# Performance work log

Measured on AMD Instinct MI355X. Metric: run time of the kernel, lower is better.

## Reference

```python
import jax, jax.numpy as jnp
import numpy as np

BN_EPS = 1e-5

@jax.custom_vjp
def bsign(x):
    # forward: sign(x) (torch semantics: sign(0)=0, matched by jnp.sign)
    return jnp.sign(x)

def _bsign_fwd(x):
    return jnp.sign(x), x

def _bsign_bwd(x, g):
    # straight-through estimator: pass grad where |x| <= 1, zero elsewhere
    return (g * (jnp.abs(x) <= 1.0).astype(g.dtype),)

bsign.defvjp(_bsign_fwd, _bsign_bwd)


def setup_inputs() -> dict:
    key = jax.random.key(0)
    k1, k2 = jax.random.split(key, 2)
    B, IN, OUT = 8192, 2048, 2048
    x = jax.random.normal(k1, (B, IN), dtype=jnp.float32)
    weight = jax.random.normal(k2, (OUT, IN), dtype=jnp.float32) * 0.1
    gamma = jnp.ones((OUT,), dtype=jnp.float32)
    beta = jnp.zeros((OUT,), dtype=jnp.float32)
    return {"x": x, "weight": weight, "gamma": gamma, "beta": beta}


def reference(x, weight, gamma, beta):
    # binarize input and weight to {-1, 0, +1} via sign (STE in bwd)
    xb = bsign(x)            # [B, IN]
    wb = bsign(weight)       # [OUT, IN]
    out = xb @ wb.T          # [B, OUT] full-precision GEMM over +/-1 values
    # BatchNorm1d, training mode: normalize with biased batch statistics
    mean = jnp.mean(out, axis=0)                 # [OUT]
    var = jnp.var(out, axis=0)                   # biased (ddof=0), matches torch BN
    out = (out - mean) * jax.lax.rsqrt(var + BN_EPS) * gamma + beta
    return out
```

## Files before the change

kernel.cpp:

```cpp
#include <hip/hip_runtime.h>
#include <stdint.h>


typedef int int32x4 __attribute__((ext_vector_type(4)));
typedef int int32x16 __attribute__((ext_vector_type(16)));

#define BM 256
#define BN 256
#define BKI 128
#define EPS_BN 1e-5f
#define BAR_STRIDE 32

__device__ __forceinline__ void load16_lds(const void* g, void* l) {
  __builtin_amdgcn_global_load_lds(
      (const __attribute__((address_space(1))) void*)g,
      (__attribute__((address_space(3))) void*)l,
      16, 0, 0);
}

__device__ __forceinline__ char sgn(float v) {
  return v > 0.f ? (char)1 : (v < 0.f ? (char)-1 : (char)0);
}

__global__ void binarize_kernel(const float* __restrict__ x,
                                const float* __restrict__ w,
                                char* __restrict__ Ab, char* __restrict__ Bb,
                                float* __restrict__ stats,
                                int nx4, int ntot4, int n2) {
  int idx = blockIdx.x * blockDim.x + threadIdx.x;
  if (idx < n2) stats[idx] = 0.f;
  if (idx >= ntot4) return;
  const float4* src;
  char* dst;
  int i;
  if (idx < nx4) {
    src = reinterpret_cast<const float4*>(x); dst = Ab; i = idx;
  } else {
    src = reinterpret_cast<const float4*>(w); dst = Bb; i = idx - nx4;
  }
  float4 v = src[i];
  char4 o;
  o.x = sgn(v.x); o.y = sgn(v.y); o.z = sgn(v.z); o.w = sgn(v.w);
  reinterpret_cast<char4*>(dst)[i] = o;
}

__global__ __launch_bounds__(512, 2) void gemm_bn_kernel(
    const char* __restrict__ A,
    const char* __restrict__ Bt,
    float* __restrict__ C,
    float* __restrict__ colSum,
    float* __restrict__ colSq,
    int* __restrict__ barriers,
    const float* __restrict__ gamma,
    const float* __restrict__ beta,
    int M, int N, int K) {
  __shared__ __align__(16) char sA[2][BM * BKI];
  __shared__ __align__(16) char sB[2][BN * BKI];

  const int tid  = threadIdx.x;
  const int wave = tid >> 6;
  const int lane = tid & 63;

  const int nby = M / BM;
  const int panel = blockIdx.x / nby;
  const int rowBlock = (blockIdx.x % nby) * BM;
  const int colBlock = panel * BN;

  const int laneRow = lane >> 3;
  const int cch     = lane & 7;
  int swzj[4];
#pragma unroll
  for (int j = 0; j < 4; ++j) swzj[j] = ((cch ^ laneRow ^ j) & 7) * 16;

  const char* Ag = A  + (size_t)(rowBlock + wave * 32 + laneRow) * K;
  const char* Bg = Bt + (size_t)(colBlock + wave * 32 + laneRow) * K;

  const int lane31 = lane & 31;
  const int hi     = lane >> 5;
  const int r2     = (lane31 >> 3) & 3;
  const int wm = (wave >> 2) * 128;
  const int wn = (wave & 3) * 64;

  int32x16 acc[4][2] = {};

  const int NT = K / BKI;

#pragma unroll
  for (int j = 0; j < 4; ++j) {
    load16_lds(Ag + (size_t)(j * 8) * K + swzj[j],
               &sA[0][(wave * 32 + j * 8) * BKI]);
    load16_lds(Bg + (size_t)(j * 8) * K + swzj[j],
               &sB[0][(wave * 32 + j * 8) * BKI]);
  }

  for (int t = 0; t < NT; ++t) {
    const int cur = t & 1;
    const int nxt = cur ^ 1;
    const char* sAc = sA[cur];
    const char* sBc = sB[cur];
    const size_t gkn = (size_t)(t + 1) * BKI;
    const bool pre = (t + 1 < NT);

    __syncthreads();

    int32x16 bf_[2];
    int32x4* bfv = reinterpret_cast<int32x4*>(&bf_[0]);
#pragma unroll
    for (int ni = 0; ni < 2; ++ni) {
      const int row = wn + ni * 32 + lane31;
#pragma unroll
      for (int ks = 0; ks < 4; ++ks) {
        const int chunk = (((ks * 2 + hi) ^ (row & 7) ^ r2) & 7) * 16;
        bfv[ni * 4 + ks] = *reinterpret_cast<const int32x4*>(
            &sBc[row * BKI + chunk]);
      }
    }

#pragma unroll
    for (int q = 0; q < 4; ++q) {
      int32x4 af[4];
      const int arow = wm + q * 32 + lane31;
#pragma unroll
      for (int ks = 0; ks < 4; ++ks) {
        const int chunk = (((ks * 2 + hi) ^ (arow & 7) ^ r2) & 7) * 16;
        af[ks] = *reinterpret_cast<const int32x4*>(&sAc[arow * BKI + chunk]);
      }

      if (pre) {
        if (q < 2) {
#pragma unroll
          for (int j = 0; j < 2; ++j) {
            const int part = q * 2 + j;
            load16_lds(Ag + gkn + (size_t)(part * 8) * K + swzj[part],
                       &sA[nxt][(wave * 32 + part * 8) * BKI]);
          }
        } else {
#pragma unroll
          for (int j = 0; j < 2; ++j) {
            const int part = (q - 2) * 2 + j;
            load16_lds(Bg + gkn + (size_t)(part * 8) * K + swzj[part],
                       &sB[nxt][(wave * 32 + part * 8) * BKI]);
          }
        }
      }

      __builtin_amdgcn_s_barrier();
      __builtin_amdgcn_s_setprio(1);
#pragma unroll
      for (int ks = 0; ks < 4; ++ks)
#pragma unroll
        for (int ni = 0; ni < 2; ++ni)
          acc[q][ni] = __builtin_amdgcn_mfma_i32_32x32x32_i8(
              af[ks], bfv[ni * 4 + ks], acc[q][ni], 0, 0, 0);
      __builtin_amdgcn_s_setprio(0);
      __builtin_amdgcn_s_barrier();
    }
  }

#pragma unroll
  for (int ni = 0; ni < 2; ++ni) {
    const int col = colBlock + wn + ni * 32 + lane31;
    float s = 0.f, sq = 0.f;
#pragma unroll
    for (int mi = 0; mi < 4; ++mi)
#pragma unroll
      for (int r = 0; r < 16; ++r) {
        const float fv = (float)acc[mi][ni][r];
        s += fv;
        sq += fv * fv;
      }
    s  += __shfl_xor(s, 32);
    sq += __shfl_xor(sq, 32);
    if (hi == 0) {
      atomicAdd(&colSum[col], s);
      atomicAdd(&colSq[col], sq);
    }
  }

  float gmv = 0.f, btv = 0.f;
  if (tid < BN) {
    gmv = gamma[colBlock + tid];
    btv = beta[colBlock + tid];
  }

  __syncthreads();
  if (tid == 0) {
    int* bar = barriers + panel * BAR_STRIDE;
    __hip_atomic_fetch_add(bar, 1, __ATOMIC_RELAXED,
                           __HIP_MEMORY_SCOPE_AGENT);
    while (__hip_atomic_load(bar, __ATOMIC_RELAXED,
                             __HIP_MEMORY_SCOPE_AGENT) < nby) {
      __builtin_amdgcn_s_sleep(8);
    }
    asm volatile("" ::: "memory");
  }
  __syncthreads();

  float2* sSC = reinterpret_cast<float2*>(&sA[0][0]);
  if (tid < BN) {
    const int col = colBlock + tid;
    const float s  = __hip_atomic_load(&colSum[col], __ATOMIC_RELAXED,
                                       __HIP_MEMORY_SCOPE_AGENT);
    const float sq = __hip_atomic_load(&colSq[col], __ATOMIC_RELAXED,
                                       __HIP_MEMORY_SCOPE_AGENT);
    const float invM = 1.0f / (float)M;
    const float mu  = s * invM;
    const float var = sq * invM - mu * mu;
    const float sc  = gmv * rsqrtf(var + EPS_BN);
    const float sh  = btv - mu * sc;
    sSC[tid] = make_float2(sc, sh);
  }
  __syncthreads();

#pragma unroll
  for (int ni = 0; ni < 2; ++ni) {
    const int lc  = wn + ni * 32 + lane31;
    const float2 ss = sSC[lc];
    const int col = colBlock + lc;
#pragma unroll
    for (int mi = 0; mi < 4; ++mi) {
#pragma unroll
      for (int r = 0; r < 16; ++r) {
        const int row = rowBlock + wm + mi * 32 + (r & 3) + 8 * (r >> 2) +
                        4 * hi;
        C[(size_t)row * N + col] = (float)acc[mi][ni][r] * ss.x + ss.y;
      }
    }
  }
}

extern "C" void kernel_launch(void* const* d_in, const int* in_sizes, int n_in,
                              void* d_out, int out_size, void* d_ws,
                              size_t ws_size, hipStream_t stream) {
  const float* x     = (const float*)d_in[0];
  const float* w     = (const float*)d_in[1];
  const float* gamma = (const float*)d_in[2];
  const float* beta  = (const float*)d_in[3];
  float* C = (float*)d_out;

  const int N = in_sizes[2];
  const int K = in_sizes[1] / N;
  const int M = in_sizes[0] / K;

  char* ws = (char*)d_ws;
  char* Abin = ws;
  char* Bbin = ws + (size_t)M * K;
  float* stats = (float*)(ws + (size_t)M * K + (size_t)N * K);
  float* colSum = stats;
  float* colSq  = stats + N;
  int* barriers = (int*)(stats + 2 * N);

  {
    int nx4 = (M * K) / 4;
    int ntot4 = (M * K + N * K) / 4;
    binarize_kernel<<<(ntot4 + 255) / 256, 256, 0, stream>>>(
        x, w, Abin, Bbin, stats, nx4, ntot4, 2 * N + 16 * BAR_STRIDE);
  }

  {
    const int nTiles = (M / BM) * (N / BN);
    gemm_bn_kernel<<<nTiles, 512, 0, stream>>>(Abin, Bbin, C, colSum, colSq,
                                               barriers, gamma, beta, M, N, K);
  }
}
```

Before: 161.8 us.

## Pack signs as FP4 and use scaled FP4 MFMA for binary GEMM

Binarization now packs eight sign values into a 32-bit word as e2m1 FP4 codes instead of int8 bytes. The GEMM uses the gfx950 scaled f8f6f4 MFMA in FP4 mode with unit scales and fp32 accumulation, halving the K-loop iterations and operand traffic. Results stay exact since sums of ±1 fit in fp32, at the cost of depending on the fp4 operand layout being right.

Measured after the change: 149.8 us. 1.08x faster.

```diff
diff --git a/kernel.cpp b/kernel.cpp
--- a/kernel.cpp
+++ b/kernel.cpp
@@ -3,13 +3,15 @@
 
 
 typedef int int32x4 __attribute__((ext_vector_type(4)));
-typedef int int32x16 __attribute__((ext_vector_type(16)));
+typedef int int32x8 __attribute__((ext_vector_type(8)));
+typedef float f32x16 __attribute__((ext_vector_type(16)));
 
 #define BM 256
 #define BN 256
 #define BKI 128
 #define EPS_BN 1e-5f
 #define BAR_STRIDE 32
+#define SCALE_ONE 0x7F7F7F7F
 
 __device__ __forceinline__ void load16_lds(const void* g, void* l) {
   __builtin_amdgcn_global_load_lds(
@@ -18,30 +20,39 @@
       16, 0, 0);
 }
 
-__device__ __forceinline__ char sgn(float v) {
-  return v > 0.f ? (char)1 : (v < 0.f ? (char)-1 : (char)0);
+__device__ __forceinline__ int32x8 mk8(int32x4 v) {
+  int32x8 r = {v[0], v[1], v[2], v[3], 0, 0, 0, 0};
+  return r;
+}
+
+__device__ __forceinline__ unsigned enc4(float v) {
+  return v > 0.f ? 2u : (v < 0.f ? 10u : 0u);
 }
 
 __global__ void binarize_kernel(const float* __restrict__ x,
                                 const float* __restrict__ w,
-                                char* __restrict__ Ab, char* __restrict__ Bb,
+                                unsigned* __restrict__ Ab,
+                                unsigned* __restrict__ Bb,
                                 float* __restrict__ stats,
-                                int nx4, int ntot4, int n2) {
+                                int nx8, int ntot8, int n2) {
   int idx = blockIdx.x * blockDim.x + threadIdx.x;
   if (idx < n2) stats[idx] = 0.f;
-  if (idx >= ntot4) return;
+  if (idx >= ntot8) return;
   const float4* src;
-  char* dst;
+  unsigned* dst;
   int i;
-  if (idx < nx4) {
+  if (idx < nx8) {
     src = reinterpret_cast<const float4*>(x); dst = Ab; i = idx;
   } else {
-    src = reinterpret_cast<const float4*>(w); dst = Bb; i = idx - nx4;
-  }
-  float4 v = src[i];
-  char4 o;
-  o.x = sgn(v.x); o.y = sgn(v.y); o.z = sgn(v.z); o.w = sgn(v.w);
-  reinterpret_cast<char4*>(dst)[i] = o;
+    src = reinterpret_cast<const float4*>(w); dst = Bb; i = idx - nx8;
+  }
+  const float4 s0 = src[2 * i];
+  const float4 s1 = src[2 * i + 1];
+  unsigned out = enc4(s0.x)        | (enc4(s0.y) << 4)  |
+                 (enc4(s0.z) << 8) | (enc4(s0.w) << 12) |
+                 (enc4(s1.x) << 16)| (enc4(s1.y) << 20) |
+                 (enc4(s1.z) << 24)| (enc4(s1.w) << 28);
+  dst[i] = out;
 }
 
 __global__ __launch_bounds__(512, 2) void gemm_bn_kernel(
@@ -60,6 +71,7 @@
   const int tid  = threadIdx.x;
   const int wave = tid >> 6;
   const int lane = tid & 63;
+  const int Kb   = K >> 1;
 
   const int nby = M / BM;
   const int panel = blockIdx.x / nby;
@@ -72,8 +84,8 @@
 #pragma unroll
   for (int j = 0; j < 4; ++j) swzj[j] = ((cch ^ laneRow ^ j) & 7) * 16;
 
-  const char* Ag = A  + (size_t)(rowBlock + wave * 32 + laneRow) * K;
-  const char* Bg = Bt + (size_t)(colBlock + wave * 32 + laneRow) * K;
+  const char* Ag = A  + (size_t)(rowBlock + wave * 32 + laneRow) * Kb;
+  const char* Bg = Bt + (size_t)(colBlock + wave * 32 + laneRow) * Kb;
 
   const int lane31 = lane & 31;
   const int hi     = lane >> 5;
@@ -81,15 +93,15 @@
   const int wm = (wave >> 2) * 128;
   const int wn = (wave & 3) * 64;
 
-  int32x16 acc[4][2] = {};
-
-  const int NT = K / BKI;
+  f32x16 acc[4][2] = {};
+
+  const int NT = Kb / BKI;
 
 #pragma unroll
   for (int j = 0; j < 4; ++j) {
-    load16_lds(Ag + (size_t)(j * 8) * K + swzj[j],
+    load16_lds(Ag + (size_t)(j * 8) * Kb + swzj[j],
                &sA[0][(wave * 32 + j * 8) * BKI]);
-    load16_lds(Bg + (size_t)(j * 8) * K + swzj[j],
+    load16_lds(Bg + (size_t)(j * 8) * Kb + swzj[j],
                &sB[0][(wave * 32 + j * 8) * BKI]);
   }
 
@@ -103,8 +115,7 @@
 
     __syncthreads();
 
-    int32x16 bf_[2];
-    int32x4* bfv = reinterpret_cast<int32x4*>(&bf_[0]);
+    int32x4 bfv[8];
 #pragma unroll
     for (int ni = 0; ni < 2; ++ni) {
       const int row = wn + ni * 32 + lane31;
@@ -131,14 +142,14 @@
 #pragma unroll
           for (int j = 0; j < 2; ++j) {
             const int part = q * 2 + j;
-            load16_lds(Ag + gkn + (size_t)(part * 8) * K + swzj[part],
+            load16_lds(Ag + gkn + (size_t)(part * 8) * Kb + swzj[part],
                        &sA[nxt][(wave * 32 + part * 8) * BKI]);
           }
         } else {
 #pragma unroll
           for (int j = 0; j < 2; ++j) {
             const int part = (q - 2) * 2 + j;
-            load16_lds(Bg + gkn + (size_t)(part * 8) * K + swzj[part],
+            load16_lds(Bg + gkn + (size_t)(part * 8) * Kb + swzj[part],
                        &sB[nxt][(wave * 32 + part * 8) * BKI]);
           }
         }
@@ -150,8 +161,11 @@
       for (int ks = 0; ks < 4; ++ks)
 #pragma unroll
         for (int ni = 0; ni < 2; ++ni)
-          acc[q][ni] = __builtin_amdgcn_mfma_i32_32x32x32_i8(
-              af[ks], bfv[ni * 4 + ks], acc[q][ni], 0, 0, 0);
+          acc[q][ni] = __builtin_amdgcn_mfma_scale_f32_32x32x64_f8f6f4(
+              mk8(af[ks]), mk8(bfv[ni * 4 + ks]), acc[q][ni],
+              4, 4,
+              0, SCALE_ONE,
+              0, SCALE_ONE);
       __builtin_amdgcn_s_setprio(0);
       __builtin_amdgcn_s_barrier();
     }
@@ -165,7 +179,7 @@
     for (int mi = 0; mi < 4; ++mi)
 #pragma unroll
       for (int r = 0; r < 16; ++r) {
-        const float fv = (float)acc[mi][ni][r];
+        const float fv = acc[mi][ni][r];
         s += fv;
         sq += fv * fv;
       }
@@ -223,7 +237,7 @@
       for (int r = 0; r < 16; ++r) {
         const int row = rowBlock + wm + mi * 32 + (r & 3) + 8 * (r >> 2) +
                         4 * hi;
-        C[(size_t)row * N + col] = (float)acc[mi][ni][r] * ss.x + ss.y;
+        C[(size_t)row * N + col] = acc[mi][ni][r] * ss.x + ss.y;
       }
     }
   }
@@ -244,17 +258,18 @@
 
   char* ws = (char*)d_ws;
   char* Abin = ws;
-  char* Bbin = ws + (size_t)M * K;
-  float* stats = (float*)(ws + (size_t)M * K + (size_t)N * K);
+  char* Bbin = ws + (size_t)M * K / 2;
+  float* stats = (float*)(ws + (size_t)M * K / 2 + (size_t)N * K / 2);
   float* colSum = stats;
   float* colSq  = stats + N;
   int* barriers = (int*)(stats + 2 * N);
 
   {
-    int nx4 = (M * K) / 4;
-    int ntot4 = (M * K + N * K) / 4;
-    binarize_kernel<<<(ntot4 + 255) / 256, 256, 0, stream>>>(
-        x, w, Abin, Bbin, stats, nx4, ntot4, 2 * N + 16 * BAR_STRIDE);
+    int nx8 = (M * K) / 8;
+    int ntot8 = (M * K + N * K) / 8;
+    binarize_kernel<<<(ntot8 + 255) / 256, 256, 0, stream>>>(
+        x, w, (unsigned*)Abin, (unsigned*)Bbin, stats, nx8, ntot8,
+        2 * N + 16 * BAR_STRIDE);
   }
 
   {
```
